# Optimization experiments

Hardware: AMD Instinct MI355X
Metric: run time of the kernel (lower is better)

The kernel has to match this reference:

```python
import jax, jax.numpy as jnp
import numpy as np

B, L, E, H = 2, 2048, 1024, 16
D = E // H  # head dim = 64


def setup_inputs() -> dict:
    key = jax.random.key(0)
    ks = jax.random.split(key, 10)
    s = 0.02
    return {
        "xt": jax.random.normal(ks[0], (B, L, E), jnp.float32),
        "xs": jax.random.normal(ks[1], (B, L, E), jnp.float32),
        "Wt": jax.random.normal(ks[2], (E, 3 * E), jnp.float32) * s,  # t_attn weight (x @ Wt)
        "bt": jnp.zeros((3 * E,), jnp.float32),
        "Ws": jax.random.normal(ks[3], (E, 2 * E), jnp.float32) * s,  # s_attn weight
        "bs": jnp.zeros((2 * E,), jnp.float32),
        "Wc": jax.random.normal(ks[4], (E, E), jnp.float32) * s,      # c_proj weight
        "bc": jnp.zeros((E,), jnp.float32),
        "lam_ts": jnp.ones((1,), jnp.float32),
        "lam_st": jnp.ones((1,), jnp.float32),
        "lam_ss": jnp.ones((1,), jnp.float32),
    }


def _heads(x):
    # (B, L, E) -> (B, H, L, D)
    return x.reshape(B, L, H, D).transpose(0, 2, 1, 3)


def reference(xt, xs, Wt, bt, Ws, bs, Wc, bc, lam_ts, lam_st, lam_ss):
    qt, kt, vt = jnp.split(xt @ Wt + bt, 3, axis=2)
    qs, ks = jnp.split(xs @ Ws + bs, 2, axis=2)
    qt, kt, vt, qs, ks = map(_heads, (qt, kt, vt, qs, ks))

    # 4-way disentangled scores; fuse the 4 matmuls into 2 by combining keys:
    # qt@kt^T + lam_ts*qt@ks^T = qt @ (kt + lam_ts*ks)^T
    # lam_st*qs@kt^T + lam_ss*qs@ks^T = qs @ (lam_st*kt + lam_ss*ks)^T
    k1 = kt + lam_ts[0] * ks
    k2 = lam_st[0] * kt + lam_ss[0] * ks
    att = (jnp.einsum('bhqd,bhkd->bhqk', qt, k1)
           + jnp.einsum('bhqd,bhkd->bhqk', qs, k2)) * (1.0 / np.sqrt(D))
    att = jax.nn.softmax(att, axis=-1)
    y = jnp.einsum('bhqk,bhkd->bhqd', att, vt)  # (B, H, L, D)
    y = y.transpose(0, 2, 1, 3).reshape(B, L, E)
    return y @ Wc + bc
```

## Files before the change

### kernel.cpp

```cpp
#include <hip/hip_runtime.h>
#include <math.h>

#define LQ 2048
#define EQ 1024
#define M_ROWS 4096
#define BH 32

typedef _Float16 f16x8 __attribute__((ext_vector_type(8)));
typedef _Float16 f16x4 __attribute__((ext_vector_type(4)));
typedef _Float16 f16x2 __attribute__((ext_vector_type(2)));
typedef float f32x4 __attribute__((ext_vector_type(4)));
typedef float f32x16 __attribute__((ext_vector_type(16)));

#define QSCALE 0.1803368801111204f
#define DEFER_THR 8.0f

__device__ __forceinline__ void async_ld16(const _Float16* g, _Float16* l) {
  __builtin_amdgcn_global_load_lds(
      (const __attribute__((address_space(1))) unsigned int*)g,
      (__attribute__((address_space(3))) unsigned int*)l, 16, 0, 0);
}

__global__ __launch_bounds__(256) void prep(
    const float* __restrict__ xt, const float* __restrict__ xs,
    const float* __restrict__ Wt, const float* __restrict__ Ws,
    const float* __restrict__ Wc,
    _Float16* __restrict__ xt16, _Float16* __restrict__ xs16,
    _Float16* __restrict__ WtT, _Float16* __restrict__ WsT,
    _Float16* __restrict__ WcT) {
  int gb = blockIdx.x;
  if (gb < 4096) {
    int i = gb * 256 + threadIdx.x;
    const float* s; _Float16* d; size_t off;
    if (i < 524288) { s = xt; d = xt16; off = (size_t)i * 8; }
    else            { s = xs; d = xs16; off = (size_t)(i - 524288) * 8; }
    float4 a = *(const float4*)&s[off];
    float4 b = *(const float4*)&s[off + 4];
    f16x8 h;
    h[0] = (_Float16)a.x; h[1] = (_Float16)a.y; h[2] = (_Float16)a.z; h[3] = (_Float16)a.w;
    h[4] = (_Float16)b.x; h[5] = (_Float16)b.y; h[6] = (_Float16)b.z; h[7] = (_Float16)b.w;
    *(f16x8*)&d[off] = h;
  } else {
    __shared__ float T[32][65];
    int tb = gb - 4096;
    int c0 = (tb % 96) * 64;
    int k0 = (tb / 96) * 32;
    const float* W; _Float16* D; int Nw, cl;
    if (c0 < 3072)      { W = Wt; D = WtT; Nw = 3072; cl = c0; }
    else if (c0 < 5120) { W = Ws; D = WsT; Nw = 2048; cl = c0 - 3072; }
    else                { W = Wc; D = WcT; Nw = 1024; cl = c0 - 5120; }
    const int tid = threadIdx.x;
#pragma unroll
    for (int p = 0; p < 4; ++p) {
      int idx = tid + p * 256;
      int row = idx >> 5;
      int c2 = (idx & 31) * 2;
      float2 v = *(const float2*)&W[(size_t)(k0 + row) * Nw + cl + c2];
      T[row][c2] = v.x;
      T[row][c2 + 1] = v.y;
    }
    __syncthreads();
#pragma unroll
    for (int p = 0; p < 4; ++p) {
      int idx = tid + p * 256;
      int col = idx >> 4;
      int k2 = (idx & 15) * 2;
      f16x2 h2;
      h2[0] = (_Float16)T[k2][col];
      h2[1] = (_Float16)T[k2 + 1][col];
      *(f16x2*)&D[(size_t)(cl + col) * 1024 + k0 + k2] = h2;
    }
  }
}

__global__ __launch_bounds__(256, 3) void proj_gemm(
    const _Float16* __restrict__ xt16, const _Float16* __restrict__ xs16,
    const _Float16* __restrict__ WtT, const _Float16* __restrict__ WsT,
    const float* __restrict__ bt, const float* __restrict__ bs,
    _Float16* __restrict__ q16, _Float16* __restrict__ k16,
    _Float16* __restrict__ v16) {
  __shared__ _Float16 Al0[128 * 32];
  __shared__ _Float16 Bl0[128 * 32];
  __shared__ _Float16 Al1[128 * 32];
  __shared__ _Float16 Bl1[128 * 32];

  const int tid = threadIdx.x;
  const int w = tid >> 6;
  const int lane = tid & 63;
  const int quad = lane >> 4;
  const int l15 = lane & 15;
  const int wm = w >> 1, wn = w & 1;
  const int by = blockIdx.y;
  const int n0 = blockIdx.x * 128;

  const _Float16* Ab;
  const _Float16* Bb;
  const float* bias;
  int m0, bsel = 0, branch;
  if (by < 32) {
    branch = 0; Ab = xt16; Bb = WtT; bias = bt; m0 = by * 128;
  } else if (by < 48) {
    branch = 1;
    int by2 = by - 32;
    bsel = by2 >> 3;
    m0 = (by2 & 7) * 128;
    Ab = WtT + (size_t)2048 * 1024;
    Bb = xt16 + (size_t)bsel * 2048 * 1024;
    bias = bt;
  } else {
    branch = 2; Ab = xs16; Bb = WsT; bias = bs; m0 = (by - 48) * 128;
  }

  const int srow = lane >> 2;
  const int schunk = ((lane & 3) ^ ((lane >> 3) & 3)) * 8;
  const int key = (l15 >> 1) & 3;

  f32x4 acc[4][4];
#pragma unroll
  for (int mb = 0; mb < 4; ++mb)
#pragma unroll
    for (int nb = 0; nb < 4; ++nb) acc[mb][nb] = (f32x4){0.f, 0.f, 0.f, 0.f};

  auto dma = [&](int kt, _Float16* Al, _Float16* Bl) {
#pragma unroll
    for (int i = 0; i < 2; ++i) {
      int rt = w * 32 + i * 16;
      async_ld16(&Ab[(size_t)(m0 + rt + srow) * 1024 + kt + schunk], &Al[rt * 32]);
      async_ld16(&Bb[(size_t)(n0 + rt + srow) * 1024 + kt + schunk], &Bl[rt * 32]);
    }
  };

  auto comp = [&](const _Float16* Al, const _Float16* Bl) {
    f16x8 af[4], bf[4];
    const int pc = (quad ^ key) * 8;
#pragma unroll
    for (int mb = 0; mb < 4; ++mb)
      af[mb] = *(const f16x8*)&Al[(wm * 64 + mb * 16 + l15) * 32 + pc];
#pragma unroll
    for (int nb = 0; nb < 4; ++nb)
      bf[nb] = *(const f16x8*)&Bl[(wn * 64 + nb * 16 + l15) * 32 + pc];
#pragma unroll
    for (int mb = 0; mb < 4; ++mb)
#pragma unroll
      for (int nb = 0; nb < 4; ++nb)
        acc[mb][nb] = __builtin_amdgcn_mfma_f32_16x16x32_f16(bf[nb], af[mb], acc[mb][nb], 0, 0, 0);
  };

  dma(0, Al0, Bl0);
  for (int kt = 0; kt < 1024; kt += 64) {
    __syncthreads();
    dma(kt + 32, Al1, Bl1);
    comp(Al0, Bl0);
    __syncthreads();
    if (kt + 64 < 1024) dma(kt + 64, Al0, Bl0);
    comp(Al1, Bl1);
  }

#pragma unroll
  for (int nb = 0; nb < 4; ++nb) {
    const int col0 = n0 + wn * 64 + nb * 16 + quad * 4;
    float4 bv4;
    if (branch != 1) bv4 = *(const float4*)&bias[col0];
#pragma unroll
    for (int mb = 0; mb < 4; ++mb) {
      int row = m0 + wm * 64 + mb * 16 + l15;
      if (branch == 1) {
        float bv = bias[2048 + row];
        f16x4 o4;
#pragma unroll
        for (int r = 0; r < 4; ++r) o4[r] = (_Float16)(acc[mb][nb][r] + bv);
        *(f16x4*)&v16[(size_t)(bsel * 1024 + row) * 2048 + col0] = o4;
      } else {
        f16x4 o4;
        o4[0] = (_Float16)(acc[mb][nb][0] + bv4.x);
        o4[1] = (_Float16)(acc[mb][nb][1] + bv4.y);
        o4[2] = (_Float16)(acc[mb][nb][2] + bv4.z);
        o4[3] = (_Float16)(acc[mb][nb][3] + bv4.w);
        int bb = row >> 11, ll = row & 2047;
        int which = col0 >> 10, e = col0 & 1023;
        int hh = e >> 6, dd = e & 63;
        size_t rowhd = (size_t)(bb * 16 + hh) * 2048 + ll;
        int off = (branch == 0) ? 0 : 64;
        _Float16* dst = (which == 0) ? q16 : k16;
        *(f16x4*)&dst[rowhd * 128 + off + dd] = o4;
      }
    }
  }
}

__global__ __launch_bounds__(256, 3) void cproj_gemm(
    const _Float16* __restrict__ A, const _Float16* __restrict__ Bm,
    const float* __restrict__ bias, float* __restrict__ outf) {
  __shared__ _Float16 Al0[128 * 32];
  __shared__ _Float16 Bl0[64 * 32];
  __shared__ _Float16 Al1[128 * 32];
  __shared__ _Float16 Bl1[64 * 32];

  const int tid = threadIdx.x;
  const int w = tid >> 6;
  const int lane = tid & 63;
  const int quad = lane >> 4;
  const int l15 = lane & 15;
  const int wm = w >> 1, wn = w & 1;
  const int m0 = blockIdx.y * 128;
  const int n0 = blockIdx.x * 64;

  const int srow = lane >> 2;
  const int schunk = ((lane & 3) ^ ((lane >> 3) & 3)) * 8;

  f32x4 acc[4][2];
#pragma unroll
  for (int mb = 0; mb < 4; ++mb)
#pragma unroll
    for (int nb = 0; nb < 2; ++nb) acc[mb][nb] = (f32x4){0.f, 0.f, 0.f, 0.f};

  const int key = (l15 >> 1) & 3;

  auto dma = [&](int kt, _Float16* Al, _Float16* Bl) {
#pragma unroll
    for (int i = 0; i < 2; ++i) {
      int rt = w * 32 + i * 16;
      async_ld16(&A[(size_t)(m0 + rt + srow) * 1024 + kt + schunk], &Al[rt * 32]);
    }
    int rtb = w * 16;
    async_ld16(&Bm[(size_t)(n0 + rtb + srow) * 1024 + kt + schunk], &Bl[rtb * 32]);
  };

  auto comp = [&](const _Float16* Al, const _Float16* Bl) {
    f16x8 af[4], bf[2];
    const int pc = (quad ^ key) * 8;
#pragma unroll
    for (int mb = 0; mb < 4; ++mb)
      af[mb] = *(const f16x8*)&Al[(wm * 64 + mb * 16 + l15) * 32 + pc];
#pragma unroll
    for (int nb = 0; nb < 2; ++nb)
      bf[nb] = *(const f16x8*)&Bl[(wn * 32 + nb * 16 + l15) * 32 + pc];
#pragma unroll
    for (int mb = 0; mb < 4; ++mb)
#pragma unroll
      for (int nb = 0; nb < 2; ++nb)
        acc[mb][nb] = __builtin_amdgcn_mfma_f32_16x16x32_f16(bf[nb], af[mb], acc[mb][nb], 0, 0, 0);
  };

  dma(0, Al0, Bl0);
  for (int kt = 0; kt < 1024; kt += 64) {
    __syncthreads();
    dma(kt + 32, Al1, Bl1);
    comp(Al0, Bl0);
    __syncthreads();
    if (kt + 64 < 1024) dma(kt + 64, Al0, Bl0);
    comp(Al1, Bl1);
  }

#pragma unroll
  for (int nb = 0; nb < 2; ++nb) {
    const int col0 = n0 + wn * 32 + nb * 16 + quad * 4;
    const float4 bv4 = *(const float4*)&bias[col0];
#pragma unroll
    for (int mb = 0; mb < 4; ++mb) {
      int row = m0 + wm * 64 + mb * 16 + l15;
      float4 o4;
      o4.x = acc[mb][nb][0] + bv4.x;
      o4.y = acc[mb][nb][1] + bv4.y;
      o4.z = acc[mb][nb][2] + bv4.z;
      o4.w = acc[mb][nb][3] + bv4.w;
      *(float4*)&outf[(size_t)row * 1024 + col0] = o4;
    }
  }
}

__global__ __launch_bounds__(256, 2) void flash_attn_mfma(
    const _Float16* __restrict__ qcat, const _Float16* __restrict__ kcat,
    const _Float16* __restrict__ vT, _Float16* __restrict__ y,
    const float* __restrict__ lam_ts, const float* __restrict__ lam_st,
    const float* __restrict__ lam_ss) {
  const int bh = blockIdx.y;
  const int qt0 = blockIdx.x * 128;
  const int b = bh >> 4, h = bh & 15;
  const _Float16* Qg = qcat + (size_t)bh * LQ * 128;
  const _Float16* Kg = kcat + (size_t)bh * LQ * 128;
  const _Float16* Vg = vT + (size_t)bh * 64 * LQ;

  __shared__ _Float16 Ksh0[64 * 128];
  __shared__ _Float16 Ksh1[64 * 128];
  __shared__ _Float16 Vsh0[64 * 64];
  __shared__ _Float16 Vsh1[64 * 64];
  __shared__ _Float16 Vsh2[64 * 64];
  __shared__ _Float16 Vsh3[64 * 64];

  const int tid = threadIdx.x;
  const int w = tid >> 6;
  const int lane = tid & 63;
  const int half = lane >> 5;
  const int l31 = lane & 31;

  const float lts = lam_ts[0], lst = lam_st[0], lss = lam_ss[0];

  f16x8 qf[8];
#pragma unroll
  for (int db = 0; db < 4; ++db) {
    const _Float16* qp = &Qg[(size_t)(qt0 + w * 32 + l31) * 128 + db * 16 + half * 8];
    f16x8 a = *(const f16x8*)qp;
    f16x8 bq = *(const f16x8*)(qp + 64);
#pragma unroll
    for (int e = 0; e < 8; ++e) {
      float fa = (float)a[e], fb = (float)bq[e];
      qf[db][e]     = (_Float16)(QSCALE * (fa + lst * fb));
      qf[db + 4][e] = (_Float16)(QSCALE * (lts * fa + lss * fb));
    }
  }

  float m_i = -INFINITY;
  float l_i = 0.f;
  f32x16 O[2];
#pragma unroll
  for (int nt = 0; nt < 2; ++nt)
#pragma unroll
    for (int r = 0; r < 16; ++r) O[nt][r] = 0.f;

  auto dma_k = [&](int t, _Float16* Kd) {
#pragma unroll
    for (int a = 0; a < 4; ++a) {
      int row = w * 16 + a * 4 + (lane >> 4);
      int sc = (lane & 15) ^ (row & 7);
      async_ld16(&Kg[(size_t)(t + row) * 128 + sc * 8], &Kd[(w * 16 + a * 4) * 128]);
    }
  };
  auto dma_v = [&](int t, _Float16* Vd) {
#pragma unroll
    for (int a = 0; a < 2; ++a) {
      int row = w * 16 + a * 8 + (lane >> 3);
      int sc = (lane & 7) ^ (row & 7);
      async_ld16(&Vg[(size_t)row * LQ + t + sc * 8], &Vd[(w * 16 + a * 8) * 64]);
    }
  };

  auto qk = [&](const _Float16* Ks, f32x16* Sp) {
    __builtin_amdgcn_s_setprio(1);
#pragma unroll
    for (int db = 0; db < 8; ++db) {
      const int pc = ((db * 2 + half) ^ (lane & 7)) * 8;
      f16x8 af0 = *(const f16x8*)&Ks[(l31) * 128 + pc];
      f16x8 af1 = *(const f16x8*)&Ks[(32 + l31) * 128 + pc];
      Sp[0] = __builtin_amdgcn_mfma_f32_32x32x16_f16(af0, qf[db], Sp[0], 0, 0, 0);
      Sp[1] = __builtin_amdgcn_mfma_f32_32x32x16_f16(af1, qf[db], Sp[1], 0, 0, 0);
    }
    __builtin_amdgcn_s_setprio(0);
  };

  auto softpv = [&](f32x16* S, const _Float16* Vs0, const _Float16* Vs1) {
    float mx = -INFINITY;
#pragma unroll
    for (int kb = 0; kb < 4; ++kb)
#pragma unroll
      for (int r = 0; r < 16; ++r) mx = fmaxf(mx, S[kb][r]);
    mx = fmaxf(mx, __shfl_xor(mx, 32));

    if (__any(mx > m_i + DEFER_THR)) {
      float m_new = fmaxf(m_i, mx);
      float alpha = __builtin_amdgcn_exp2f(m_i - m_new);
      l_i *= alpha;
#pragma unroll
      for (int nt = 0; nt < 2; ++nt)
#pragma unroll
        for (int r = 0; r < 16; ++r) O[nt][r] *= alpha;
      m_i = m_new;
    }

    float s = 0.f;
#pragma unroll
    for (int kb = 0; kb < 4; ++kb)
#pragma unroll
      for (int r = 0; r < 16; ++r) {
        float p = __builtin_amdgcn_exp2f(S[kb][r] - m_i);
        S[kb][r] = p;
        s += p;
      }
    s += __shfl_xor(s, 32);
    l_i += s;

#pragma unroll
    for (int kb = 0; kb < 4; ++kb) {
      unsigned pu[8];
#pragma unroll
      for (int i = 0; i < 8; ++i) {
        f16x2 t2;
        t2[0] = (_Float16)S[kb][2 * i];
        t2[1] = (_Float16)S[kb][2 * i + 1];
        pu[i] = __builtin_bit_cast(unsigned, t2);
      }
#pragma unroll
      for (int c = 0; c < 2; ++c) {
        unsigned u0 = pu[4 * c + 0], u1 = pu[4 * c + 1];
        unsigned u2 = pu[4 * c + 2], u3 = pu[4 * c + 3];
        asm("v_permlane32_swap_b32 %0, %1" : "+v"(u0), "+v"(u2));
        asm("v_permlane32_swap_b32 %0, %1" : "+v"(u1), "+v"(u3));
        union { unsigned u[4]; f16x8 v; } pb;
        pb.u[0] = u0; pb.u[1] = u1; pb.u[2] = u2; pb.u[3] = u3;
        const int kb2 = kb * 2 + c;
        const _Float16* Vs = (kb2 < 4) ? Vs0 : Vs1;
        const int kb2r = kb2 & 3;
        f16x8 av[2];
#pragma unroll
        for (int nt = 0; nt < 2; ++nt) {
          int dim = nt * 32 + l31;
          int pc = ((kb2r * 2 + half) ^ (dim & 7)) * 8;
          av[nt] = *(const f16x8*)&Vs[dim * 64 + pc];
        }
        __builtin_amdgcn_s_setprio(1);
#pragma unroll
        for (int nt = 0; nt < 2; ++nt)
          O[nt] = __builtin_amdgcn_mfma_f32_32x32x16_f16(av[nt], pb.v, O[nt], 0, 0, 0);
        __builtin_amdgcn_s_setprio(0);
      }
    }
  };

  auto step = [&](int t, const _Float16* Vr0, _Float16* Vr1, _Float16* Vw2) {
    f32x16 S[4];
#pragma unroll
    for (int kb = 0; kb < 4; ++kb)
#pragma unroll
      for (int r = 0; r < 16; ++r) S[kb][r] = 0.f;

    __syncthreads();
    dma_k(t + 64, Ksh1);
    dma_v(t + 64, Vr1);
    qk(Ksh0, &S[0]);
    __syncthreads();
    if (t + 128 < LQ) {
      dma_k(t + 128, Ksh0);
      dma_v(t + 128, Vw2);
    }
    qk(Ksh1, &S[2]);
    softpv(S, Vr0, Vr1);
  };

  dma_k(0, Ksh0);
  dma_v(0, Vsh0);
  for (int t = 0; t < LQ; t += 256) {
    step(t,       Vsh0, Vsh1, Vsh2);
    step(t + 128, Vsh2, Vsh3, Vsh0);
  }

  float inv = 1.f / l_i;
  int qrow = qt0 + w * 32 + l31;
#pragma unroll
  for (int nt = 0; nt < 2; ++nt)
#pragma unroll
    for (int rg = 0; rg < 4; ++rg) {
      f16x4 o4;
#pragma unroll
      for (int i = 0; i < 4; ++i) o4[i] = (_Float16)(O[nt][rg * 4 + i] * inv);
      int dim = nt * 32 + rg * 8 + half * 4;
      *(f16x4*)&y[((size_t)b * LQ + qrow) * EQ + h * 64 + dim] = o4;
    }
}

extern "C" void kernel_launch(void* const* d_in, const int* in_sizes, int n_in,
                              void* d_out, int out_size, void* d_ws, size_t ws_size,
                              hipStream_t stream) {
  const float* xt = (const float*)d_in[0];
  const float* xs = (const float*)d_in[1];
  const float* Wt = (const float*)d_in[2];
  const float* bt = (const float*)d_in[3];
  const float* Ws = (const float*)d_in[4];
  const float* bs = (const float*)d_in[5];
  const float* Wc = (const float*)d_in[6];
  const float* bc = (const float*)d_in[7];
  const float* lam_ts = (const float*)d_in[8];
  const float* lam_st = (const float*)d_in[9];
  const float* lam_ss = (const float*)d_in[10];
  float* out = (float*)d_out;

  _Float16* w16 = (_Float16*)d_ws;
  _Float16* xt16 = w16;
  _Float16* xs16 = xt16 + 4194304;
  _Float16* WtT  = xs16 + 4194304;
  _Float16* WsT  = WtT + 3145728;
  _Float16* WcT  = WsT + 2097152;
  _Float16* qcat = WcT + 1048576;
  _Float16* kcat = qcat + 8388608;
  _Float16* vbufT = kcat + 8388608;
  _Float16* ybuf = vbufT + 4194304;

  prep<<<7168, 256, 0, stream>>>(xt, xs, Wt, Ws, Wc, xt16, xs16, WtT, WsT, WcT);
  proj_gemm<<<dim3(16, 80), 256, 0, stream>>>(
      xt16, xs16, WtT, WsT, bt, bs, qcat, kcat, vbufT);
  flash_attn_mfma<<<dim3(16, 32), 256, 0, stream>>>(
      qcat, kcat, vbufT, ybuf, lam_ts, lam_st, lam_ss);
  cproj_gemm<<<dim3(16, 32), 256, 0, stream>>>(ybuf, WcT, bc, out);
}
```

Before: 266.0 us.

## Stage projection GEMM epilogue through LDS and swizzle workgroup order

The projection GEMM epilogue now writes its f16 results into a single shared LDS buffer (reusing the double-buffer space) with an XOR swizzle, then reads them back so each thread issues 16-byte coalesced global stores instead of scattered 8-byte stores. Workgroup indices are also remapped so that neighbouring workgroups cover different row blocks, which is meant to improve L2 reuse of operand tiles. This adds two barriers and an LDS round trip at the end of each tile.

Measured after the change: 262.4 us. Within noise of the previous version (-1.4%).

```diff
diff --git a/kernel.cpp b/kernel.cpp
--- a/kernel.cpp
+++ b/kernel.cpp
@@ -79,10 +79,11 @@
     const float* __restrict__ bt, const float* __restrict__ bs,
     _Float16* __restrict__ q16, _Float16* __restrict__ k16,
     _Float16* __restrict__ v16) {
-  __shared__ _Float16 Al0[128 * 32];
-  __shared__ _Float16 Bl0[128 * 32];
-  __shared__ _Float16 Al1[128 * 32];
-  __shared__ _Float16 Bl1[128 * 32];
+  __shared__ _Float16 LS[128 * 128];
+  _Float16* Al0 = LS;
+  _Float16* Bl0 = LS + 4096;
+  _Float16* Al1 = LS + 8192;
+  _Float16* Bl1 = LS + 12288;
 
   const int tid = threadIdx.x;
   const int w = tid >> 6;
@@ -90,8 +91,12 @@
   const int quad = lane >> 4;
   const int l15 = lane & 15;
   const int wm = w >> 1, wn = w & 1;
-  const int by = blockIdx.y;
-  const int n0 = blockIdx.x * 128;
+
+  const int wg = blockIdx.y * 16 + blockIdx.x;
+  const int swz = (wg & 7) * 160 + (wg >> 3);
+  const int bx = swz & 15;
+  const int by = swz >> 4;
+  const int n0 = bx * 128;
 
   const _Float16* Ab;
   const _Float16* Bb;
@@ -156,34 +161,49 @@
     comp(Al1, Bl1);
   }
 
-#pragma unroll
-  for (int nb = 0; nb < 4; ++nb) {
-    const int col0 = n0 + wn * 64 + nb * 16 + quad * 4;
-    float4 bv4;
-    if (branch != 1) bv4 = *(const float4*)&bias[col0];
-#pragma unroll
-    for (int mb = 0; mb < 4; ++mb) {
-      int row = m0 + wm * 64 + mb * 16 + l15;
+  __syncthreads();
+#pragma unroll
+  for (int mb = 0; mb < 4; ++mb) {
+    const int rowL = wm * 64 + mb * 16 + l15;
+    const int rx = (rowL & 7) << 3;
+    float rbias = 0.f;
+    if (branch == 1) rbias = bias[2048 + m0 + rowL];
+#pragma unroll
+    for (int nb = 0; nb < 4; ++nb) {
+      const int colL = wn * 64 + nb * 16 + quad * 4;
+      f16x4 o4;
       if (branch == 1) {
-        float bv = bias[2048 + row];
-        f16x4 o4;
-#pragma unroll
-        for (int r = 0; r < 4; ++r) o4[r] = (_Float16)(acc[mb][nb][r] + bv);
-        *(f16x4*)&v16[(size_t)(bsel * 1024 + row) * 2048 + col0] = o4;
+#pragma unroll
+        for (int r = 0; r < 4; ++r) o4[r] = (_Float16)(acc[mb][nb][r] + rbias);
       } else {
-        f16x4 o4;
+        const float4 bv4 = *(const float4*)&bias[n0 + colL];
         o4[0] = (_Float16)(acc[mb][nb][0] + bv4.x);
         o4[1] = (_Float16)(acc[mb][nb][1] + bv4.y);
         o4[2] = (_Float16)(acc[mb][nb][2] + bv4.z);
         o4[3] = (_Float16)(acc[mb][nb][3] + bv4.w);
-        int bb = row >> 11, ll = row & 2047;
-        int which = col0 >> 10, e = col0 & 1023;
-        int hh = e >> 6, dd = e & 63;
-        size_t rowhd = (size_t)(bb * 16 + hh) * 2048 + ll;
-        int off = (branch == 0) ? 0 : 64;
-        _Float16* dst = (which == 0) ? q16 : k16;
-        *(f16x4*)&dst[rowhd * 128 + off + dd] = o4;
       }
+      *(f16x4*)&LS[rowL * 128 + (colL ^ rx)] = o4;
+    }
+  }
+  __syncthreads();
+
+  const int g = tid & 15;
+  const int c8 = g * 8;
+#pragma unroll
+  for (int p = 0; p < 8; ++p) {
+    const int r = p * 16 + (tid >> 4);
+    f16x8 v8 = *(const f16x8*)&LS[r * 128 + (c8 ^ ((r & 7) << 3))];
+    if (branch == 1) {
+      *(f16x8*)&v16[(size_t)(bsel * 1024 + m0 + r) * 2048 + n0 + c8] = v8;
+    } else {
+      const int grow = m0 + r;
+      const int col = n0 + c8;
+      const int bb = grow >> 11, ll = grow & 2047;
+      const int which = col >> 10, e = col & 1023;
+      const int hh = e >> 6, dd = e & 63;
+      _Float16* dst = which ? k16 : q16;
+      const int off = (branch == 0) ? 0 : 64;
+      *(f16x8*)&dst[((size_t)(bb * 16 + hh) * 2048 + ll) * 128 + off + dd] = v8;
     }
   }
 }
```
